# Optimization experiments

Hardware: AMD Instinct MI355X
Metric: run time of the kernel (lower is better)

The kernel has to match this reference:

```python
import jax, jax.numpy as jnp
import numpy as np

N_NODES = 50000
N_EDGES = 400000
IN_C, HID, EDGE_D = 128, 256, 32
NUM_LAYERS = 3

def _gnblock(x, src, dst, edge_attr, ew, eb, nw, nb):
    # edge message MLP: relu(W [x_src, x_dst, e] + b)  -> [E, HID]
    m = jax.nn.relu(jnp.concatenate([x[src], x[dst], edge_attr], axis=-1) @ ew + eb)
    # mean aggregation by destination node
    agg = jax.ops.segment_sum(m, dst, num_segments=N_NODES)
    deg = jax.ops.segment_sum(jnp.ones((m.shape[0],), m.dtype), dst, num_segments=N_NODES)
    agg = agg / jnp.maximum(deg, 1.0)[:, None]
    # node update MLP: relu(W [x, agg] + b) -> [N, HID]
    return jax.nn.relu(jnp.concatenate([x, agg], axis=-1) @ nw + nb)

def setup_inputs() -> dict:
    key = jax.random.key(0)
    ks = jax.random.split(key, 12)
    s = 0.05  # keep activations sane
    return {
        'x': jax.random.normal(ks[0], (N_NODES, IN_C), jnp.float32),
        'edge_index': jax.random.randint(ks[1], (2, N_EDGES), 0, N_NODES, jnp.int32),
        'edge_attr': jax.random.normal(ks[2], (N_EDGES, EDGE_D), jnp.float32),
        'e0_w': jax.random.normal(ks[3], (2 * IN_C + EDGE_D, HID), jnp.float32) * s,
        'e0_b': jnp.zeros((HID,), jnp.float32),
        'n0_w': jax.random.normal(ks[4], (IN_C + HID, HID), jnp.float32) * s,
        'n0_b': jnp.zeros((HID,), jnp.float32),
        'e_w': jax.random.normal(ks[5], (NUM_LAYERS - 1, 2 * HID + EDGE_D, HID), jnp.float32) * s,
        'e_b': jnp.zeros((NUM_LAYERS - 1, HID), jnp.float32),
        'n_w': jax.random.normal(ks[6], (NUM_LAYERS - 1, 2 * HID, HID), jnp.float32) * s,
        'n_b': jnp.zeros((NUM_LAYERS - 1, HID), jnp.float32),
        'h1_w': jax.random.normal(ks[7], (HID, HID), jnp.float32) * s,
        'h1_b': jnp.zeros((HID,), jnp.float32),
        'h2_w': jax.random.normal(ks[8], (HID, 1), jnp.float32) * s,
        'h2_b': jnp.zeros((1,), jnp.float32),
    }

def reference(x, edge_index, edge_attr, e0_w, e0_b, n0_w, n0_b,
              e_w, e_b, n_w, n_b, h1_w, h1_b, h2_w, h2_b):
    src, dst = edge_index[0], edge_index[1]
    h = _gnblock(x, src, dst, edge_attr, e0_w, e0_b, n0_w, n0_b)
    for i in range(NUM_LAYERS - 1):
        h = _gnblock(h, src, dst, edge_attr, e_w[i], e_b[i], n_w[i], n_b[i])
    # MLP head -> per-node logit [N, 1]
    h = jax.nn.relu(h @ h1_w + h1_b)
    return h @ h2_w + h2_b
```

## Files before the change

### kernel.cpp

```cpp
#include <hip/hip_runtime.h>
#include <hip/hip_bf16.h>
#include <hip/hip_fp16.h>

#define NN 50000
#define NE 400000
#define NBLK 196
#define PST 544

typedef unsigned short u16;
typedef unsigned int u32;
typedef __attribute__((ext_vector_type(8))) short short8;
typedef __attribute__((ext_vector_type(4))) float f32x4;
typedef __attribute__((ext_vector_type(4))) unsigned short u16x4;
typedef __attribute__((ext_vector_type(2))) _Float16 h2;
typedef __attribute__((ext_vector_type(2))) unsigned int u32x2;

typedef __attribute__((address_space(1))) const void as1_void;
typedef __attribute__((address_space(3))) void as3_void;

static __device__ __forceinline__ float bf2f(u16 u) {
    return __uint_as_float(((u32)u) << 16);
}
static __device__ __forceinline__ float bf2f_lo(u32 u) {
    return __uint_as_float(u << 16);
}
static __device__ __forceinline__ float bf2f_hi(u32 u) {
    return __uint_as_float(u & 0xffff0000u);
}
static __device__ __forceinline__ u16 f2bf(float f) {
    u32 x = __float_as_uint(f);
    x += 0x7fffu + ((x >> 16) & 1u);
    return (u16)(x >> 16);
}
static __device__ __forceinline__ u32 packbf2(float a, float b) {
    return ((u32)f2bf(b) << 16) | (u32)f2bf(a);
}
static __device__ __forceinline__ u32 packh2(float a, float b) {
    return ((u32)__half_as_ushort(__float2half(b)) << 16) |
           (u32)__half_as_ushort(__float2half(a));
}

static __device__ __forceinline__ void gload_lds16(const u16* g, u16* l) {
    __builtin_amdgcn_global_load_lds((as1_void*)g, (as3_void*)l, 16, 0, 0);
}

#define DOT8(ea, wA, wB, wC, wD)                                        \
    asm("v_dot2_f32_f16 %0, %2, %6, %0\n\t"                             \
        "v_dot2_f32_f16 %1, %2, %7, %1\n\t"                             \
        "v_dot2_f32_f16 %0, %3, %8, %0\n\t"                             \
        "v_dot2_f32_f16 %1, %3, %9, %1\n\t"                             \
        "v_dot2_f32_f16 %0, %4, %10, %0\n\t"                            \
        "v_dot2_f32_f16 %1, %4, %11, %1\n\t"                            \
        "v_dot2_f32_f16 %0, %5, %12, %0\n\t"                            \
        "v_dot2_f32_f16 %1, %5, %13, %1\n\t"                            \
        : "+v"(q0), "+v"(q1)                                            \
        : "s"(ea.x), "s"(ea.y), "s"(ea.z), "s"(ea.w),                   \
          "v"(wA.x), "v"(wA.y), "v"(wB.x), "v"(wB.y),                   \
          "v"(wC.x), "v"(wC.y), "v"(wD.x), "v"(wD.y))

__global__ __launch_bounds__(256) void gemm_bt(
    const u16* __restrict__ A, int lda,
    const u16* __restrict__ Bt,
    u16* __restrict__ C, int ldc,
    int M, int K,
    const float* __restrict__ bias,
    int relu)
{
    __shared__ u16 As[128 * 32];
    __shared__ u16 Bs[128 * 32];

    const int t = threadIdx.x;
    const int w = t >> 6;
    const int lane = t & 63;
    const int quad = lane >> 4;
    const int l15 = lane & 15;
    const int tile_m = blockIdx.x * 128;
    const int tile_n = blockIdx.y * 128;
    const int wm = (w >> 1) * 64;
    const int wn = (w & 1) * 64;

    f32x4 acc[4][4];
#pragma unroll
    for (int r = 0; r < 4; ++r)
#pragma unroll
        for (int c = 0; c < 4; ++c)
            acc[r][c] = (f32x4){0.f, 0.f, 0.f, 0.f};

    int ar0 = tile_m + (t >> 2);      if (ar0 > M - 1) ar0 = M - 1;
    int ar1 = tile_m + 64 + (t >> 2); if (ar1 > M - 1) ar1 = M - 1;
    const int br0 = tile_n + (t >> 2);
    const int br1 = tile_n + 64 + (t >> 2);
    const int koff = (t & 3) * 8;

    u16* lAs0 = As + w * 512;
    u16* lAs1 = As + 2048 + w * 512;
    u16* lBs0 = Bs + w * 512;
    u16* lBs1 = Bs + 2048 + w * 512;

    const u16* Arow0 = A + (size_t)ar0 * lda + koff;
    const u16* Arow1 = A + (size_t)ar1 * lda + koff;
    const u16* Brow0 = Bt + (size_t)br0 * K + koff;
    const u16* Brow1 = Bt + (size_t)br1 * K + koff;

    for (int k0 = 0; k0 < K; k0 += 32) {
        gload_lds16(Arow0 + k0, lAs0);
        gload_lds16(Arow1 + k0, lAs1);
        gload_lds16(Brow0 + k0, lBs0);
        gload_lds16(Brow1 + k0, lBs1);
        __syncthreads();

        short8 af[4], bfr[4];
#pragma unroll
        for (int r = 0; r < 4; ++r)
            af[r] = *(const short8*)&As[(wm + r * 16 + l15) * 32 + quad * 8];
#pragma unroll
        for (int c = 0; c < 4; ++c)
            bfr[c] = *(const short8*)&Bs[(wn + c * 16 + l15) * 32 + quad * 8];
#pragma unroll
        for (int r = 0; r < 4; ++r)
#pragma unroll
            for (int c = 0; c < 4; ++c)
                acc[r][c] = __builtin_amdgcn_mfma_f32_16x16x32_bf16(af[r], bfr[c], acc[r][c], 0, 0, 0);
        __syncthreads();
    }

#pragma unroll
    for (int r = 0; r < 4; ++r) {
#pragma unroll
        for (int c = 0; c < 4; ++c) {
            const int coln = tile_n + wn + c * 16 + l15;
            const float bv = bias ? bias[coln] : 0.0f;
#pragma unroll
            for (int i = 0; i < 4; ++i) {
                const int row = tile_m + wm + r * 16 + quad * 4 + i;
                if (row < M) {
                    float v = acc[r][c][i] + bv;
                    if (relu) v = fmaxf(v, 0.f);
                    C[(size_t)row * ldc + coln] = f2bf(v);
                }
            }
        }
    }
}

__global__ __launch_bounds__(256)
__attribute__((amdgpu_waves_per_eu(1)))
void edge_agg_fused(
    const u16* __restrict__ P,
    const u32* __restrict__ eattr_p32,
    const u32* __restrict__ WePk,
    const int* __restrict__ row_start,
    const int* __restrict__ src_perm,
    const float* __restrict__ inv_deg,
    u16* __restrict__ aggZ)
{
    const int wid = (int)((blockIdx.x * 256 + threadIdx.x) >> 6);
    const int node = wid >> 1;
    const int half = wid & 1;
    const int lane = threadIdx.x & 63;
    const int coff = half * 128 + lane * 2;
    if (node >= NN) return;

    const u32* wb0  = WePk + 0 * 256 + coff;
    const u32* wb4  = WePk + 4 * 256 + coff;
    const u32* wb8  = WePk + 8 * 256 + coff;
    const u32* wb12 = WePk + 12 * 256 + coff;
    u32x2 w0, w1, w2, w3, w4, w5, w6, w7, w8, w9, w10, w11, w12, w13, w14, w15;
    asm volatile("global_load_dwordx2 %0, %1, off"             : "=v"(w0)  : "v"(wb0));
    asm volatile("global_load_dwordx2 %0, %1, off offset:1024" : "=v"(w1)  : "v"(wb0));
    asm volatile("global_load_dwordx2 %0, %1, off offset:2048" : "=v"(w2)  : "v"(wb0));
    asm volatile("global_load_dwordx2 %0, %1, off offset:3072" : "=v"(w3)  : "v"(wb0));
    asm volatile("global_load_dwordx2 %0, %1, off"             : "=v"(w4)  : "v"(wb4));
    asm volatile("global_load_dwordx2 %0, %1, off offset:1024" : "=v"(w5)  : "v"(wb4));
    asm volatile("global_load_dwordx2 %0, %1, off offset:2048" : "=v"(w6)  : "v"(wb4));
    asm volatile("global_load_dwordx2 %0, %1, off offset:3072" : "=v"(w7)  : "v"(wb4));
    asm volatile("global_load_dwordx2 %0, %1, off"             : "=v"(w8)  : "v"(wb8));
    asm volatile("global_load_dwordx2 %0, %1, off offset:1024" : "=v"(w9)  : "v"(wb8));
    asm volatile("global_load_dwordx2 %0, %1, off offset:2048" : "=v"(w10) : "v"(wb8));
    asm volatile("global_load_dwordx2 %0, %1, off offset:3072" : "=v"(w11) : "v"(wb8));
    asm volatile("global_load_dwordx2 %0, %1, off"             : "=v"(w12) : "v"(wb12));
    asm volatile("global_load_dwordx2 %0, %1, off offset:1024" : "=v"(w13) : "v"(wb12));
    asm volatile("global_load_dwordx2 %0, %1, off offset:2048" : "=v"(w14) : "v"(wb12));
    asm volatile("global_load_dwordx2 %0, %1, off offset:3072" : "=v"(w15) : "v"(wb12));

    const u32 pdu = *(const u32*)(P + (size_t)node * PST + 256 + coff);
    const float pb0 = bf2f_lo(pdu);
    const float pb1 = bf2f_hi(pdu);

    asm volatile("s_waitcnt vmcnt(0)" ::: "memory");

    float acc0 = 0.f, acc1 = 0.f;
    const int s0r = row_start[node], s1r = row_start[node + 1];

    if (s1r > s0r) {
        const int jlast = s1r - 1;
        int j1 = (s0r + 1 < jlast) ? s0r + 1 : jlast;

        int ja = __builtin_amdgcn_readfirstlane(s0r);
        int jb = __builtin_amdgcn_readfirstlane(j1);
        int sa = src_perm[ja];
        int sb = src_perm[jb];
        u32 psa = *(const u32*)(P + (size_t)sa * PST + coff);
        u32 psb = *(const u32*)(P + (size_t)sb * PST + coff);
        const uint4* epa = (const uint4*)(eattr_p32 + (size_t)ja * 16);
        const uint4* epb = (const uint4*)(eattr_p32 + (size_t)jb * 16);
        uint4 ea0 = epa[0], ea1 = epa[1], ea2 = epa[2], ea3 = epa[3];
        uint4 eb0 = epb[0], eb1 = epb[1], eb2 = epb[2], eb3 = epb[3];

        for (int j = s0r; j < s1r; ++j) {
            int jc = (j + 2 < jlast) ? j + 2 : jlast;
            int jcs = __builtin_amdgcn_readfirstlane(jc);
            int sn = src_perm[jcs];
            u32 psn = *(const u32*)(P + (size_t)sn * PST + coff);
            const uint4* epn = (const uint4*)(eattr_p32 + (size_t)jcs * 16);
            uint4 en0 = epn[0], en1 = epn[1], en2 = epn[2], en3 = epn[3];

            float q0 = pb0, q1 = pb1;
            DOT8(ea0, w0, w1, w2, w3);
            DOT8(ea1, w4, w5, w6, w7);
            DOT8(ea2, w8, w9, w10, w11);
            DOT8(ea3, w12, w13, w14, w15);

            q0 += bf2f_lo(psa);
            q1 += bf2f_hi(psa);
            acc0 += fmaxf(q0, 0.f);
            acc1 += fmaxf(q1, 0.f);

            psa = psb; psb = psn;
            ea0 = eb0; ea1 = eb1; ea2 = eb2; ea3 = eb3;
            eb0 = en0; eb1 = en1; eb2 = en2; eb3 = en3;
        }
    }

    const float idg = inv_deg[node];
    *(u32*)(aggZ + (size_t)node * 512 + coff) = packbf2(acc0 * idg, acc1 * idg);
}

__global__ __launch_bounds__(256) void head_out(
    const u16* __restrict__ h4Z,
    const float* __restrict__ h2w,
    const float* __restrict__ h2b,
    float* __restrict__ out)
{
    const int node = (int)((blockIdx.x * 256 + threadIdx.x) >> 6);
    const int lane = threadIdx.x & 63;
    if (node >= NN) return;
    const int col = lane * 4;
    u16x4 hv = *(const u16x4*)(h4Z + (size_t)node * 512 + col);
    float4 wv = *(const float4*)(h2w + col);
    float s = bf2f(hv[0]) * wv.x + bf2f(hv[1]) * wv.y +
              bf2f(hv[2]) * wv.z + bf2f(hv[3]) * wv.w;
    for (int off = 32; off > 0; off >>= 1)
        s += __shfl_down(s, off, 64);
    if (lane == 0) out[node] = s + h2b[0];
}

__global__ void zero_int(int* p, int n) {
    int i = blockIdx.x * 256 + threadIdx.x;
    if (i < n) p[i] = 0;
}

__global__ void hist_k(const int* __restrict__ ei, int* __restrict__ deg) {
    int e = blockIdx.x * 256 + threadIdx.x;
    if (e < NE) atomicAdd(&deg[ei[NE + e]], 1);
}

__global__ __launch_bounds__(256) void block_sum_k(const int* __restrict__ deg,
                                                   int* __restrict__ bsum) {
    __shared__ int sm[4];
    const int i = blockIdx.x * 256 + threadIdx.x;
    int v = (i < NN) ? deg[i] : 0;
    for (int off = 32; off > 0; off >>= 1)
        v += __shfl_down(v, off, 64);
    const int lane = threadIdx.x & 63;
    const int w = threadIdx.x >> 6;
    if (lane == 0) sm[w] = v;
    __syncthreads();
    if (threadIdx.x == 0)
        bsum[blockIdx.x] = sm[0] + sm[1] + sm[2] + sm[3];
}

__global__ __launch_bounds__(256) void scan_block_k(const int* __restrict__ bsum,
                                                    int* __restrict__ boff,
                                                    int* __restrict__ row_start) {
    __shared__ int sm[256];
    const int tid = threadIdx.x;
    int v = (tid < NBLK) ? bsum[tid] : 0;
    sm[tid] = v;
    __syncthreads();
    for (int o = 1; o < 256; o <<= 1) {
        int tv = (tid >= o) ? sm[tid - o] : 0;
        __syncthreads();
        sm[tid] += tv;
        __syncthreads();
    }
    if (tid < NBLK) boff[tid] = sm[tid] - v;
    if (tid == NBLK - 1) row_start[NN] = sm[tid];
}

__global__ __launch_bounds__(256) void writeback_k(const int* __restrict__ deg,
                                                   const int* __restrict__ boff,
                                                   int* __restrict__ row_start,
                                                   int* __restrict__ cursor,
                                                   float* __restrict__ inv_deg) {
    __shared__ int sm[256];
    const int tid = threadIdx.x;
    const int i = blockIdx.x * 256 + tid;
    int v = (i < NN) ? deg[i] : 0;
    sm[tid] = v;
    __syncthreads();
    for (int o = 1; o < 256; o <<= 1) {
        int tv = (tid >= o) ? sm[tid - o] : 0;
        __syncthreads();
        sm[tid] += tv;
        __syncthreads();
    }
    if (i < NN) {
        const int rs = boff[blockIdx.x] + sm[tid] - v;
        row_start[i] = rs;
        cursor[i]    = rs;
        inv_deg[i]   = 1.0f / fmaxf((float)v, 1.0f);
    }
}

__global__ void scatter_k(const int* __restrict__ ei, const float* __restrict__ eattr,
                          int* __restrict__ cursor, int* __restrict__ src_perm,
                          u32* __restrict__ eattr_p32) {
    int e = blockIdx.x * 256 + threadIdx.x;
    if (e >= NE) return;
    int s = ei[e], d = ei[NE + e];
    int pos = atomicAdd(&cursor[d], 1);
    src_perm[pos] = s;
    const float* sr = eattr + (size_t)e * 32;
    u32 pk[16];
#pragma unroll
    for (int j = 0; j < 16; ++j)
        pk[j] = packh2(sr[2 * j], sr[2 * j + 1]);
    uint4* dr = (uint4*)(eattr_p32 + (size_t)pos * 16);
    dr[0] = (uint4){pk[0], pk[1], pk[2], pk[3]};
    dr[1] = (uint4){pk[4], pk[5], pk[6], pk[7]};
    dr[2] = (uint4){pk[8], pk[9], pk[10], pk[11]};
    dr[3] = (uint4){pk[12], pk[13], pk[14], pk[15]};
}

__global__ void bias_build(const float* __restrict__ e0b,
                           const float* __restrict__ eb1,
                           const float* __restrict__ eb2,
                           float* __restrict__ dst) {
    int i = blockIdx.x * 256 + threadIdx.x;
    if (i >= 1536) return;
    int l = i >> 9, c = i & 511;
    const float* s = (l == 0) ? e0b : (l == 1) ? eb1 : eb2;
    dst[i] = (c < 256) ? 0.f : s[c - 256];
}

struct TJob { const float* src; u16* dst; int K; int ksh; int tr; int dstride; };
struct TJobs { TJob j[16]; };

__global__ void transpose_k(TJobs jobs) {
    TJob jb = jobs.j[blockIdx.y];
    int idx = blockIdx.x * 256 + threadIdx.x;
    if (idx >= (jb.K << 8)) return;
    if (jb.tr == 1) {
        int n = idx >> jb.ksh;
        int k = idx & (jb.K - 1);
        jb.dst[n * jb.dstride + k] = f2bf(jb.src[k * 256 + n]);
    } else {
        int kp = idx >> 8;
        int c = idx & 255;
        ((u32*)jb.dst)[idx] = packh2(jb.src[(2 * kp) * 256 + c],
                                     jb.src[(2 * kp + 1) * 256 + c]);
    }
}

__global__ void cvt_x(const float* __restrict__ src, u16* __restrict__ Z) {
    int i = blockIdx.x * 256 + threadIdx.x;
    if (i >= NN * 128) return;
    int n = i >> 7, c = i & 127;
    Z[(size_t)n * 512 + 256 + c] = f2bf(src[i]);
}

extern "C" void kernel_launch(void* const* d_in, const int* in_sizes, int n_in,
                              void* d_out, int out_size, void* d_ws, size_t ws_size,
                              hipStream_t stream) {
    const float* x     = (const float*)d_in[0];
    const int*   ei    = (const int*)d_in[1];
    const float* eattr = (const float*)d_in[2];
    const float* e0_w  = (const float*)d_in[3];
    const float* e0_b  = (const float*)d_in[4];
    const float* n0_w  = (const float*)d_in[5];
    const float* n0_b  = (const float*)d_in[6];
    const float* e_w   = (const float*)d_in[7];
    const float* e_b   = (const float*)d_in[8];
    const float* n_w   = (const float*)d_in[9];
    const float* n_b   = (const float*)d_in[10];
    const float* h1_w  = (const float*)d_in[11];
    const float* h1_b  = (const float*)d_in[12];
    const float* h2_w  = (const float*)d_in[13];
    const float* h2_b  = (const float*)d_in[14];
    float* out = (float*)d_out;
    (void)in_sizes; (void)n_in; (void)out_size; (void)ws_size;

    char* base = (char*)d_ws;
    size_t off = 0;
    auto alloc = [&](size_t nbytes) -> void* {
        void* p = base + off;
        off += (nbytes + 255) & ~(size_t)255;
        return p;
    };

    int*   deg       = (int*)alloc(NN * 4);
    int*   row_start = (int*)alloc((NN + 1) * 4);
    int*   cursor    = (int*)alloc(NN * 4);
    float* invdeg    = (float*)alloc(NN * 4);
    int*   bsum      = (int*)alloc(NBLK * 4);
    int*   boff      = (int*)alloc(NBLK * 4);
    int*   src_perm  = (int*)alloc(NE * 4);
    u32*   eattr_p32 = (u32*)alloc((size_t)NE * 16 * 4);
    u16*   WcatT0    = (u16*)alloc(512 * 128 * 2);
    u16*   WcatT1    = (u16*)alloc(512 * 256 * 2);
    u16*   WcatT2    = (u16*)alloc(512 * 256 * 2);
    u32*   WePk0     = (u32*)alloc(16 * 256 * 4);
    u32*   WePk1     = (u32*)alloc(16 * 256 * 4);
    u32*   WePk2     = (u32*)alloc(16 * 256 * 4);
    u16*   BcatT0    = (u16*)alloc(256 * 384 * 2);
    u16*   BcatT1    = (u16*)alloc(256 * 512 * 2);
    u16*   BcatT2    = (u16*)alloc(256 * 512 * 2);
    u16*   H1T       = (u16*)alloc(256 * 256 * 2);
    float* bias512   = (float*)alloc(3 * 512 * 4);
    u16*   P         = (u16*)alloc((size_t)NN * PST * 2);
    u16*   Z0        = (u16*)alloc((size_t)NN * 512 * 2);
    u16*   Z1        = (u16*)alloc((size_t)NN * 512 * 2);

    zero_int<<<(NN + 255) / 256, 256, 0, stream>>>(deg, NN);
    hist_k<<<(NE + 255) / 256, 256, 0, stream>>>(ei, deg);
    block_sum_k<<<NBLK, 256, 0, stream>>>(deg, bsum);
    scan_block_k<<<1, 256, 0, stream>>>(bsum, boff, row_start);
    writeback_k<<<NBLK, 256, 0, stream>>>(deg, boff, row_start, cursor, invdeg);
    scatter_k<<<(NE + 255) / 256, 256, 0, stream>>>(ei, eattr, cursor, src_perm, eattr_p32);
    bias_build<<<6, 256, 0, stream>>>(e0_b, e_b, e_b + 256, bias512);

    const float* ew2 = e_w + 544 * 256;
    const float* nw2 = n_w + 512 * 256;

    TJobs tj;
    auto setj = [&](int i, const float* s, void* d, int K, int tr, int dstride) {
        tj.j[i].src = s; tj.j[i].dst = (u16*)d; tj.j[i].K = K; tj.j[i].tr = tr;
        tj.j[i].dstride = dstride;
        tj.j[i].ksh = (K == 256) ? 8 : (K == 128 ? 7 : 5);
    };
    setj(0,  e0_w,             WcatT0,             128, 1, 128);
    setj(1,  e0_w + 128 * 256, WcatT0 + 256 * 128, 128, 1, 128);
    setj(2,  e_w,              WcatT1,             256, 1, 256);
    setj(3,  e_w + 256 * 256,  WcatT1 + 256 * 256, 256, 1, 256);
    setj(4,  ew2,              WcatT2,             256, 1, 256);
    setj(5,  ew2 + 256 * 256,  WcatT2 + 256 * 256, 256, 1, 256);
    setj(6,  n0_w + 128 * 256, BcatT0,             256, 1, 384);
    setj(7,  n0_w,             BcatT0 + 256,       128, 1, 384);
    setj(8,  n_w + 256 * 256,  BcatT1,             256, 1, 512);
    setj(9,  n_w,              BcatT1 + 256,       256, 1, 512);
    setj(10, nw2 + 256 * 256,  BcatT2,             256, 1, 512);
    setj(11, nw2,              BcatT2 + 256,       256, 1, 512);
    setj(12, h1_w,             H1T,                256, 1, 256);
    setj(13, e0_w + 256 * 256, WePk0,              16,  2, 0);
    setj(14, e_w + 512 * 256,  WePk1,              16,  2, 0);
    setj(15, ew2 + 512 * 256,  WePk2,              16,  2, 0);
    transpose_k<<<dim3(256, 16), 256, 0, stream>>>(tj);

    cvt_x<<<(NN * 128 + 255) / 256, 256, 0, stream>>>(x, Z0);

    const int MT = (NN + 127) / 128;
    const int AGG_BLK = (2 * NN) / 4;
    u16* WcatT[3] = {WcatT0, WcatT1, WcatT2};
    u32* WePk[3]  = {WePk0, WePk1, WePk2};
    u16* BcatT[3] = {BcatT0, BcatT1, BcatT2};
    const float* nbs[3] = {n0_b, n_b, n_b + 256};
    u16* Zin[3]  = {Z0, Z1, Z0};
    u16* Zout[3] = {Z1, Z0, Z1};
    const int kin[3]   = {128, 256, 256};
    const int knode[3] = {384, 512, 512};

    for (int l = 0; l < 3; ++l) {
        gemm_bt<<<dim3(MT, 4), 256, 0, stream>>>(Zin[l] + 256, 512, WcatT[l], P, PST,
                                                 NN, kin[l], bias512 + l * 512, 0);
        edge_agg_fused<<<AGG_BLK, 256, 0, stream>>>(P, eattr_p32, WePk[l], row_start,
                                                    src_perm, invdeg, Zin[l]);
        gemm_bt<<<dim3(MT, 2), 256, 0, stream>>>(Zin[l], 512, BcatT[l], Zout[l] + 256, 512,
                                                 NN, knode[l], nbs[l], 1);
    }
    gemm_bt<<<dim3(MT, 2), 256, 0, stream>>>(Z1 + 256, 512, H1T, Z1, 512,
                                             NN, 256, h1_b, 1);
    head_out<<<NN / 4, 256, 0, stream>>>(Z1, h2_w, h2_b, out);
}
```

Measured before the change: 808.3 us.

## Unroll edge loop by four with deeper prefetch and vector-operand dots

Restructures the per-node edge aggregation loop to process four edges per iteration with four in-flight prefetch slots instead of a rolling two-deep prefetch, masking the tail edges with a multiplier. The edge attributes are now fed to v_dot2 as VGPR operands rather than scalar registers, and the waves_per_eu(1) occupancy restriction is removed. The aim is to hide gather latency for P rows and edge attributes through more outstanding loads and higher occupancy. The cost is extra register pressure from four attribute slots, and wasted dot work on padded tail edges for low-degree nodes.

```diff
diff --git a/kernel.cpp b/kernel.cpp
--- a/kernel.cpp
+++ b/kernel.cpp
@@ -44,7 +44,7 @@
     __builtin_amdgcn_global_load_lds((as1_void*)g, (as3_void*)l, 16, 0, 0);
 }
 
-#define DOT8(ea, wA, wB, wC, wD)                                        \
+#define DOT8V(ea, wA, wB, wC, wD)                                       \
     asm("v_dot2_f32_f16 %0, %2, %6, %0\n\t"                             \
         "v_dot2_f32_f16 %1, %2, %7, %1\n\t"                             \
         "v_dot2_f32_f16 %0, %3, %8, %0\n\t"                             \
@@ -54,7 +54,7 @@
         "v_dot2_f32_f16 %0, %5, %12, %0\n\t"                            \
         "v_dot2_f32_f16 %1, %5, %13, %1\n\t"                            \
         : "+v"(q0), "+v"(q1)                                            \
-        : "s"(ea.x), "s"(ea.y), "s"(ea.z), "s"(ea.w),                   \
+        : "v"(ea.x), "v"(ea.y), "v"(ea.z), "v"(ea.w),                   \
           "v"(wA.x), "v"(wA.y), "v"(wB.x), "v"(wB.y),                   \
           "v"(wC.x), "v"(wC.y), "v"(wD.x), "v"(wD.y))
 
@@ -143,9 +143,7 @@
     }
 }
 
-__global__ __launch_bounds__(256)
-__attribute__((amdgpu_waves_per_eu(1)))
-void edge_agg_fused(
+__global__ __launch_bounds__(256) void edge_agg_fused(
     const u16* __restrict__ P,
     const u32* __restrict__ eattr_p32,
     const u32* __restrict__ WePk,
@@ -194,42 +192,53 @@
 
     if (s1r > s0r) {
         const int jlast = s1r - 1;
-        int j1 = (s0r + 1 < jlast) ? s0r + 1 : jlast;
-
-        int ja = __builtin_amdgcn_readfirstlane(s0r);
-        int jb = __builtin_amdgcn_readfirstlane(j1);
-        int sa = src_perm[ja];
-        int sb = src_perm[jb];
-        u32 psa = *(const u32*)(P + (size_t)sa * PST + coff);
-        u32 psb = *(const u32*)(P + (size_t)sb * PST + coff);
-        const uint4* epa = (const uint4*)(eattr_p32 + (size_t)ja * 16);
-        const uint4* epb = (const uint4*)(eattr_p32 + (size_t)jb * 16);
-        uint4 ea0 = epa[0], ea1 = epa[1], ea2 = epa[2], ea3 = epa[3];
-        uint4 eb0 = epb[0], eb1 = epb[1], eb2 = epb[2], eb3 = epb[3];
-
-        for (int j = s0r; j < s1r; ++j) {
-            int jc = (j + 2 < jlast) ? j + 2 : jlast;
-            int jcs = __builtin_amdgcn_readfirstlane(jc);
-            int sn = src_perm[jcs];
-            u32 psn = *(const u32*)(P + (size_t)sn * PST + coff);
-            const uint4* epn = (const uint4*)(eattr_p32 + (size_t)jcs * 16);
-            uint4 en0 = epn[0], en1 = epn[1], en2 = epn[2], en3 = epn[3];
-
-            float q0 = pb0, q1 = pb1;
-            DOT8(ea0, w0, w1, w2, w3);
-            DOT8(ea1, w4, w5, w6, w7);
-            DOT8(ea2, w8, w9, w10, w11);
-            DOT8(ea3, w12, w13, w14, w15);
-
-            q0 += bf2f_lo(psa);
-            q1 += bf2f_hi(psa);
-            acc0 += fmaxf(q0, 0.f);
-            acc1 += fmaxf(q1, 0.f);
-
-            psa = psb; psb = psn;
-            ea0 = eb0; ea1 = eb1; ea2 = eb2; ea3 = eb3;
-            eb0 = en0; eb1 = en1; eb2 = en2; eb3 = en3;
+
+        u32 ps0, ps1, ps2, ps3;
+        uint4 e0a, e0b, e0c, e0d;
+        uint4 e1a, e1b, e1c, e1d;
+        uint4 e2a, e2b, e2c, e2d;
+        uint4 e3a, e3b, e3c, e3d;
+
+#define LOADSLOT(k, jj) do {                                              \
+        int js_ = __builtin_amdgcn_readfirstlane(                         \
+            ((jj) < jlast) ? (jj) : jlast);                               \
+        int ss_ = src_perm[js_];                                          \
+        ps##k = *(const u32*)(P + (size_t)ss_ * PST + coff);              \
+        const uint4* ep_ = (const uint4*)(eattr_p32 + (size_t)js_ * 16);  \
+        e##k##a = ep_[0]; e##k##b = ep_[1];                               \
+        e##k##c = ep_[2]; e##k##d = ep_[3];                               \
+    } while (0)
+
+#define CONSUME(k, jj) do {                                               \
+        float q0 = pb0, q1 = pb1;                                         \
+        DOT8V(e##k##a, w0, w1, w2, w3);                                   \
+        DOT8V(e##k##b, w4, w5, w6, w7);                                   \
+        DOT8V(e##k##c, w8, w9, w10, w11);                                 \
+        DOT8V(e##k##d, w12, w13, w14, w15);                               \
+        q0 += bf2f_lo(ps##k);                                             \
+        q1 += bf2f_hi(ps##k);                                             \
+        float m_ = ((jj) < s1r) ? 1.0f : 0.0f;                            \
+        acc0 = fmaf(m_, fmaxf(q0, 0.f), acc0);                            \
+        acc1 = fmaf(m_, fmaxf(q1, 0.f), acc1);                            \
+    } while (0)
+
+        LOADSLOT(0, s0r + 0);
+        LOADSLOT(1, s0r + 1);
+        LOADSLOT(2, s0r + 2);
+        LOADSLOT(3, s0r + 3);
+
+        for (int j = s0r; j < s1r; j += 4) {
+            CONSUME(0, j);
+            CONSUME(1, j + 1);
+            LOADSLOT(0, j + 4);
+            LOADSLOT(1, j + 5);
+            CONSUME(2, j + 2);
+            CONSUME(3, j + 3);
+            LOADSLOT(2, j + 6);
+            LOADSLOT(3, j + 7);
         }
+#undef LOADSLOT
+#undef CONSUME
     }
 
     const float idg = inv_deg[node];
```

After: 870.9 us. 7.7% more time.
